# Kernel optimization log

Measured on AMD Instinct MI355X. Metric: run time of the kernel, lower is better.

The kernel has to match this reference:

```python
import jax, jax.numpy as jnp
import numpy as np

HIDDEN = 512

def setup_inputs() -> dict:
    key = jax.random.key(0)
    kx, kq, kk, kv = jax.random.split(key, 4)
    B, S, H = 4, 4096, HIDDEN
    scale = 1.0 / np.sqrt(H)
    x = jax.random.normal(kx, (B, S, H), dtype=jnp.float32)
    # nn.Linear weights are [out, in]; y = x @ W.T
    Wq = jax.random.normal(kq, (H, H), dtype=jnp.float32) * scale
    Wk = jax.random.normal(kk, (H, H), dtype=jnp.float32) * scale
    Wv = jax.random.normal(kv, (H, H), dtype=jnp.float32) * scale
    return {"x": x, "Wq": Wq, "Wk": Wk, "Wv": Wv}

def reference(x, Wq, Wk, Wv):
    H = x.shape[-1]
    q = jnp.einsum('bsh,oh->bso', x, Wq)
    k = jnp.einsum('bsh,oh->bso', x, Wk)
    v = jnp.einsum('bsh,oh->bso', x, Wv)
    scores = jnp.einsum('bqh,bkh->bqk', q, k) / jnp.sqrt(jnp.asarray(H, x.dtype))
    att = jax.nn.softmax(scores, axis=-1)  # max-subtracted softmax, same math as manual version
    return jnp.einsum('bqk,bkh->bqh', att, v)
```

## Files before the change

kernel.cpp:

```cpp
#include <hip/hip_runtime.h>
#include <stdint.h>

typedef unsigned short u16;
typedef __bf16  bf16x8   __attribute__((ext_vector_type(8)));
typedef float   floatx4  __attribute__((ext_vector_type(4)));
typedef unsigned short ushortx4 __attribute__((ext_vector_type(4)));

__device__ __forceinline__ u16 f2bf(float f) {
  unsigned u = __builtin_bit_cast(unsigned, f);
  u += 0x7FFFu + ((u >> 16) & 1u);
  return (u16)(u >> 16);
}

#define GLD_LDS16(g, l)                                                        \
  __builtin_amdgcn_global_load_lds(                                            \
      (const __attribute__((address_space(1))) void*)(g),                      \
      (__attribute__((address_space(3))) void*)(l), 16, 0, 0)

__global__ __launch_bounds__(256) void cvt_w(
    const float* __restrict__ Wq, const float* __restrict__ Wk,
    const float* __restrict__ Wv, u16* __restrict__ dst)
{
  const int z = blockIdx.y;
  const float* src = (z == 0) ? Wq : (z == 1) ? Wk : Wv;
  u16* d = dst + (size_t)z * 262144;
  const int idx = (blockIdx.x * 256 + threadIdx.x) * 8;
  const float4 lo = *(const float4*)&src[idx];
  const float4 hi = *(const float4*)&src[idx + 4];
  union { u16 h[8]; uint4 v; } pk;
  pk.h[0] = f2bf(lo.x); pk.h[1] = f2bf(lo.y); pk.h[2] = f2bf(lo.z); pk.h[3] = f2bf(lo.w);
  pk.h[4] = f2bf(hi.x); pk.h[5] = f2bf(hi.y); pk.h[6] = f2bf(hi.z); pk.h[7] = f2bf(hi.w);
  *(uint4*)&d[idx] = pk.v;
}

__global__ __launch_bounds__(256) void cvt_x(
    const float* __restrict__ X, u16* __restrict__ dst)
{
  const int idx = (blockIdx.x * 256 + threadIdx.x) * 8;
  const float4 lo = *(const float4*)&X[idx];
  const float4 hi = *(const float4*)&X[idx + 4];
  union { u16 h[8]; uint4 v; } pk;
  pk.h[0] = f2bf(lo.x); pk.h[1] = f2bf(lo.y); pk.h[2] = f2bf(lo.z); pk.h[3] = f2bf(lo.w);
  pk.h[4] = f2bf(hi.x); pk.h[5] = f2bf(hi.y); pk.h[6] = f2bf(hi.z); pk.h[7] = f2bf(hi.w);
  *(uint4*)&dst[idx] = pk.v;
}

__global__ __launch_bounds__(256, 2) void qkv_gemm(
    const u16* __restrict__ X16, const u16* __restrict__ Wb,
    u16* __restrict__ qo, u16* __restrict__ ko, u16* __restrict__ vto)
{
  __shared__ u16 As[128 * 32];
  __shared__ u16 Bs[128 * 32];

  const int tid = threadIdx.x;
  const int w  = tid >> 6, l = tid & 63;
  const int lr = l & 15, lq = l >> 4;
  const int lk = lq * 8;
  const int m0 = blockIdx.x * 128;
  const int n0 = blockIdx.y * 128;
  const int z  = blockIdx.z;
  const u16* W = Wb + (size_t)z * 262144;
  const int wm = (w & 1) * 64, wn = (w >> 1) * 64;

  floatx4 acc[4][4];
  const floatx4 fz = {0.f, 0.f, 0.f, 0.f};
#pragma unroll
  for (int i = 0; i < 4; ++i)
#pragma unroll
    for (int j = 0; j < 4; ++j) acc[i][j] = fz;

  for (int kk = 0; kk < 512; kk += 32) {
    __syncthreads();
#pragma unroll
    for (int i = 0; i < 2; ++i) {
      const int c = i * 256 + tid;
      const int row = c >> 2, c8 = (c & 3) * 8;
      GLD_LDS16(X16 + (size_t)(m0 + row) * 512 + kk + c8, &As[c * 8]);
      GLD_LDS16(W   + (size_t)(n0 + row) * 512 + kk + c8, &Bs[c * 8]);
    }
    __syncthreads();

    bf16x8 af[4], bfr[4];
#pragma unroll
    for (int t = 0; t < 4; ++t) {
      af[t]  = *(const bf16x8*)&As[(wm + t * 16 + lr) * 32 + lk];
      bfr[t] = *(const bf16x8*)&Bs[(wn + t * 16 + lr) * 32 + lk];
    }
#pragma unroll
    for (int i = 0; i < 4; ++i)
#pragma unroll
      for (int j = 0; j < 4; ++j)
        acc[i][j] = __builtin_amdgcn_mfma_f32_16x16x32_bf16(af[i], bfr[j],
                                                            acc[i][j], 0, 0, 0);
  }

  const int cr = lq * 4;
  if (z == 2) {
#pragma unroll
    for (int i = 0; i < 4; ++i)
#pragma unroll
      for (int j = 0; j < 4; ++j) {
        const int n = n0 + wn + j * 16 + lr;
        const int m = m0 + wm + i * 16 + cr;
        ushortx4 pk;
#pragma unroll
        for (int r = 0; r < 4; ++r) pk[r] = f2bf(acc[i][j][r]);
        *(ushortx4*)&vto[(size_t)n * 16384 + m] = pk;
      }
  } else {
    u16* dst = (z == 0) ? qo : ko;
    const float sc = (z == 0) ? 0.06375871732f : 1.0f;
#pragma unroll
    for (int i = 0; i < 4; ++i)
#pragma unroll
      for (int j = 0; j < 4; ++j) {
        const int m = m0 + wm + i * 16 + cr;
        const int n = n0 + wn + j * 16 + lr;
#pragma unroll
        for (int r = 0; r < 4; ++r)
          dst[(size_t)(m + r) * 512 + n] = f2bf(acc[i][j][r] * sc);
      }
  }
}

__global__ __launch_bounds__(256, 2) void qk_exp(
    const u16* __restrict__ q, const u16* __restrict__ k,
    u16* __restrict__ S, float* __restrict__ lsum)
{
  __shared__ u16 As[128 * 32];
  __shared__ u16 Bs[128 * 32];

  const int tid = threadIdx.x;
  const int w  = tid >> 6, l = tid & 63;
  const int lr = l & 15, lq = l >> 4;
  const int lk = lq * 8;
  const int m0 = blockIdx.x * 128;
  const int n0 = blockIdx.y * 128;
  const int b  = blockIdx.z;
  const int wm = (w & 1) * 64, wn = (w >> 1) * 64;
  const size_t rb = (size_t)b * 4096;

  floatx4 acc[4][4];
  const floatx4 fz = {0.f, 0.f, 0.f, 0.f};
#pragma unroll
  for (int i = 0; i < 4; ++i)
#pragma unroll
    for (int j = 0; j < 4; ++j) acc[i][j] = fz;

  for (int kk = 0; kk < 512; kk += 32) {
    __syncthreads();
#pragma unroll
    for (int i = 0; i < 2; ++i) {
      const int c = i * 256 + tid;
      const int row = c >> 2, c8 = (c & 3) * 8;
      GLD_LDS16(k + (rb + n0 + row) * 512 + kk + c8, &As[c * 8]);
      GLD_LDS16(q + (rb + m0 + row) * 512 + kk + c8, &Bs[c * 8]);
    }
    __syncthreads();

    bf16x8 af[4], bfr[4];
#pragma unroll
    for (int t = 0; t < 4; ++t) {
      af[t]  = *(const bf16x8*)&As[(wm + t * 16 + lr) * 32 + lk];
      bfr[t] = *(const bf16x8*)&Bs[(wn + t * 16 + lr) * 32 + lk];
    }
#pragma unroll
    for (int i = 0; i < 4; ++i)
#pragma unroll
      for (int j = 0; j < 4; ++j)
        acc[i][j] = __builtin_amdgcn_mfma_f32_16x16x32_bf16(af[i], bfr[j],
                                                            acc[i][j], 0, 0, 0);
  }

  const int cr = lq * 4;
  u16* Sb = S + ((size_t)b << 24);
  float js[4] = {0.f, 0.f, 0.f, 0.f};
#pragma unroll
  for (int i = 0; i < 4; ++i)
#pragma unroll
    for (int j = 0; j < 4; ++j) {
      const int key = n0 + wm + i * 16 + cr;
      const int qr  = m0 + wn + j * 16 + lr;
      ushortx4 pk;
      float s4 = 0.f;
#pragma unroll
      for (int r = 0; r < 4; ++r) {
        const float p = __builtin_amdgcn_exp2f(acc[i][j][r] - 17.31234049f);
        s4 += p;
        pk[r] = f2bf(p);
      }
      js[j] += s4;
      *(ushortx4*)&Sb[(size_t)qr * 4096 + key] = pk;
    }
#pragma unroll
  for (int j = 0; j < 4; ++j) {
    float s = js[j];
    s += __shfl_xor(s, 16);
    s += __shfl_xor(s, 32);
    if (lq == 0)
      atomicAdd(&lsum[rb + m0 + wn + j * 16 + lr], s);
  }
}

__global__ __launch_bounds__(256, 2) void pv(
    const u16* __restrict__ S, const u16* __restrict__ vt,
    const float* __restrict__ lsum, float* __restrict__ out)
{
  __shared__ u16 As[128 * 32];
  __shared__ u16 Bs[128 * 32];

  const int tid = threadIdx.x;
  const int w  = tid >> 6, l = tid & 63;
  const int lr = l & 15, lq = l >> 4;
  const int lk = lq * 8;

  const int wg = blockIdx.x;
  const int li = (wg & 7) * 64 + (wg >> 3);
  const int n0 = (li & 3) * 128;
  const int m0 = ((li >> 2) & 31) * 128;
  const int b  = li >> 7;
  const int wm = (w & 1) * 64, wn = (w >> 1) * 64;
  const u16* Sb = S + ((size_t)b << 24);

  floatx4 acc[4][4];
  const floatx4 fz = {0.f, 0.f, 0.f, 0.f};
#pragma unroll
  for (int i = 0; i < 4; ++i)
#pragma unroll
    for (int j = 0; j < 4; ++j) acc[i][j] = fz;

  for (int kk = 0; kk < 4096; kk += 32) {
    __syncthreads();
#pragma unroll
    for (int i = 0; i < 2; ++i) {
      const int c = i * 256 + tid;
      const int row = c >> 2, c8 = (c & 3) * 8;
      GLD_LDS16(Sb + (size_t)(m0 + row) * 4096 + kk + c8, &As[c * 8]);
      GLD_LDS16(vt + (size_t)(n0 + row) * 16384 + b * 4096 + kk + c8, &Bs[c * 8]);
    }
    __syncthreads();

    bf16x8 af[4], bfr[4];
#pragma unroll
    for (int t = 0; t < 4; ++t) {
      af[t]  = *(const bf16x8*)&As[(wm + t * 16 + lr) * 32 + lk];
      bfr[t] = *(const bf16x8*)&Bs[(wn + t * 16 + lr) * 32 + lk];
    }
#pragma unroll
    for (int i = 0; i < 4; ++i)
#pragma unroll
      for (int j = 0; j < 4; ++j)
        acc[i][j] = __builtin_amdgcn_mfma_f32_16x16x32_bf16(af[i], bfr[j],
                                                            acc[i][j], 0, 0, 0);
  }

  const int cr = lq * 4;
#pragma unroll
  for (int i = 0; i < 4; ++i) {
    const int m = m0 + wm + i * 16 + cr;
    float inv[4];
#pragma unroll
    for (int r = 0; r < 4; ++r)
      inv[r] = 1.0f / lsum[(size_t)b * 4096 + m + r];
#pragma unroll
    for (int j = 0; j < 4; ++j) {
      const int n = n0 + wn + j * 16 + lr;
#pragma unroll
      for (int r = 0; r < 4; ++r)
        out[((size_t)b * 4096 + m + r) * 512 + n] = acc[i][j][r] * inv[r];
    }
  }
}

extern "C" void kernel_launch(void* const* d_in, const int* in_sizes, int n_in,
                              void* d_out, int out_size, void* d_ws, size_t ws_size,
                              hipStream_t stream) {
  (void)in_sizes; (void)n_in; (void)out_size; (void)ws_size;
  const float* x  = (const float*)d_in[0];
  const float* Wq = (const float*)d_in[1];
  const float* Wk = (const float*)d_in[2];
  const float* Wv = (const float*)d_in[3];
  float* out = (float*)d_out;
  u16* ws  = (u16*)d_ws;
  u16* qw  = ws;
  u16* kw  = qw + (size_t)16384 * 512;
  u16* vw  = kw + (size_t)16384 * 512;
  u16* x16 = vw + (size_t)16384 * 512;
  u16* wb  = x16 + (size_t)16384 * 512;
  u16* Sp  = wb + (size_t)3 * 262144;
  float* lsum = (float*)(Sp + ((size_t)4 << 24));

  hipMemsetAsync(lsum, 0, 16384 * sizeof(float), stream);
  cvt_w<<<dim3(128, 3), dim3(256), 0, stream>>>(Wq, Wk, Wv, wb);
  cvt_x<<<dim3(4096), dim3(256), 0, stream>>>(x, x16);
  qkv_gemm<<<dim3(128, 4, 3), dim3(256), 0, stream>>>(x16, wb, qw, kw, vw);
  qk_exp<<<dim3(32, 32, 4), dim3(256), 0, stream>>>(qw, kw, Sp, lsum);
  pv<<<dim3(512), dim3(256), 0, stream>>>(Sp, vw, lsum, out);
}
```

Measured before the change: 310.2 us.

## Rewrite QK-exp kernel with 256x256 tiles, 8 waves, double-buffered swizzled LDS pipeline

The score kernel moves from 128x128 tiles with 4 waves and a load/sync/compute loop to 256x256 tiles with 8 waves. K and Q are streamed into a double-buffered, XOR-swizzled 128 KB LDS region, with loads issued several stages ahead and explicit vmcnt waits, barriers and setprio around the MFMA bursts. The aim is to hide global-load latency, avoid LDS bank conflicts and raise data reuse per loaded byte. The cost is much higher register (32 accumulators) and LDS use, which lowers occupancy, and a fragile hand-written wait/barrier schedule.

```diff
diff --git a/kernel.cpp b/kernel.cpp
--- a/kernel.cpp
+++ b/kernel.cpp
@@ -123,82 +123,138 @@
   }
 }
 
-__global__ __launch_bounds__(256, 2) void qk_exp(
+__global__ __launch_bounds__(512, 2) void qk_exp8(
     const u16* __restrict__ q, const u16* __restrict__ k,
     u16* __restrict__ S, float* __restrict__ lsum)
 {
-  __shared__ u16 As[128 * 32];
-  __shared__ u16 Bs[128 * 32];
+  __shared__ u16 lds[65536];
 
   const int tid = threadIdx.x;
   const int w  = tid >> 6, l = tid & 63;
   const int lr = l & 15, lq = l >> 4;
-  const int lk = lq * 8;
-  const int m0 = blockIdx.x * 128;
-  const int n0 = blockIdx.y * 128;
-  const int b  = blockIdx.z;
-  const int wm = (w & 1) * 64, wn = (w >> 1) * 64;
+  const int wA = (w & 1) * 16;
+  const int wB = (w >> 1) * 16;
+  const int kb0 = blockIdx.x * 256;
+  const int qb0 = blockIdx.y * 256;
+  const int b   = blockIdx.z;
   const size_t rb = (size_t)b * 4096;
-
-  floatx4 acc[4][4];
+  const u16* kg = k + rb * 512;
+  const u16* qg = q + rb * 512;
+
+  floatx4 acc[8][4];
   const floatx4 fz = {0.f, 0.f, 0.f, 0.f};
 #pragma unroll
-  for (int i = 0; i < 4; ++i)
+  for (int i = 0; i < 8; ++i)
 #pragma unroll
     for (int j = 0; j < 4; ++j) acc[i][j] = fz;
 
-  for (int kk = 0; kk < 512; kk += 32) {
-    __syncthreads();
+  auto stage = [&](int s) {
+    const int ts = s >> 2, kind = s & 3;
+    const int mat = kind & 1, h = kind >> 1;
+    const u16* src = mat ? qg : kg;
+    const int rbase = mat ? qb0 : kb0;
+    u16* dst = &lds[(ts & 1) * 32768 + mat * 16384];
 #pragma unroll
     for (int i = 0; i < 2; ++i) {
-      const int c = i * 256 + tid;
-      const int row = c >> 2, c8 = (c & 3) * 8;
-      GLD_LDS16(k + (rb + n0 + row) * 512 + kk + c8, &As[c * 8]);
-      GLD_LDS16(q + (rb + m0 + row) * 512 + kk + c8, &Bs[c * 8]);
-    }
-    __syncthreads();
-
-    bf16x8 af[4], bfr[4];
-#pragma unroll
-    for (int t = 0; t < 4; ++t) {
-      af[t]  = *(const bf16x8*)&As[(wm + t * 16 + lr) * 32 + lk];
-      bfr[t] = *(const bf16x8*)&Bs[(wn + t * 16 + lr) * 32 + lk];
-    }
-#pragma unroll
-    for (int i = 0; i < 4; ++i)
-#pragma unroll
-      for (int j = 0; j < 4; ++j)
-        acc[i][j] = __builtin_amdgcn_mfma_f32_16x16x32_bf16(af[i], bfr[j],
-                                                            acc[i][j], 0, 0, 0);
+      const int c = i * 512 + tid;
+      const int r = h * 128 + (c >> 3), k16 = c & 7;
+      const int k16s = k16 ^ (r & 7);
+      GLD_LDS16(src + (size_t)(rbase + r) * 512 + ts * 64 + k16s * 8,
+                &dst[r * 64 + k16 * 8]);
+    }
+  };
+
+#pragma unroll
+  for (int s = 0; s < 6; ++s) stage(s);
+  asm volatile("s_waitcnt vmcnt(4)" ::: "memory");
+  __builtin_amdgcn_s_barrier();
+  __builtin_amdgcn_sched_barrier(0);
+
+#pragma unroll
+  for (int t = 0; t < 8; ++t) {
+#pragma unroll
+    for (int qd = 0; qd < 4; ++qd) {
+      const int fmh = qd >> 1, fnh = qd & 1;
+      const u16* AB = &lds[(t & 1) * 32768];
+      const u16* BB = AB + 16384;
+
+      bf16x8 af[4][2], bfv[2][2];
+#pragma unroll
+      for (int im = 0; im < 4; ++im) {
+        const int rA = (fmh * 4 + im) * 32 + wA + lr;
+#pragma unroll
+        for (int ks = 0; ks < 2; ++ks) {
+          const int k16p = (ks * 4 + lq) ^ (rA & 7);
+          af[im][ks] = *(const bf16x8*)&AB[rA * 64 + k16p * 8];
+        }
+      }
+#pragma unroll
+      for (int jn = 0; jn < 2; ++jn) {
+        const int rB = (fnh * 2 + jn) * 64 + wB + lr;
+#pragma unroll
+        for (int ks = 0; ks < 2; ++ks) {
+          const int k16p = (ks * 4 + lq) ^ (rB & 7);
+          bfv[jn][ks] = *(const bf16x8*)&BB[rB * 64 + k16p * 8];
+        }
+      }
+
+      const int s = t * 4 + qd + 6;
+      if (s < 32) stage(s);
+
+      __builtin_amdgcn_sched_barrier(0);
+      __builtin_amdgcn_s_barrier();
+      asm volatile("s_waitcnt lgkmcnt(0)" ::: "memory");
+      __builtin_amdgcn_sched_barrier(0);
+
+      __builtin_amdgcn_s_setprio(1);
+#pragma unroll
+      for (int im = 0; im < 4; ++im)
+#pragma unroll
+        for (int jn = 0; jn < 2; ++jn)
+#pragma unroll
+          for (int ks = 0; ks < 2; ++ks)
+            acc[fmh * 4 + im][fnh * 2 + jn] =
+                __builtin_amdgcn_mfma_f32_16x16x32_bf16(
+                    af[im][ks], bfv[jn][ks],
+                    acc[fmh * 4 + im][fnh * 2 + jn], 0, 0, 0);
+      __builtin_amdgcn_s_setprio(0);
+
+      if (qd == 3) {
+        if (t < 6)        asm volatile("s_waitcnt vmcnt(4)" ::: "memory");
+        else if (t == 6)  asm volatile("s_waitcnt vmcnt(0)" ::: "memory");
+      }
+      __builtin_amdgcn_s_barrier();
+      __builtin_amdgcn_sched_barrier(0);
+    }
   }
 
   const int cr = lq * 4;
   u16* Sb = S + ((size_t)b << 24);
   float js[4] = {0.f, 0.f, 0.f, 0.f};
 #pragma unroll
-  for (int i = 0; i < 4; ++i)
-#pragma unroll
-    for (int j = 0; j < 4; ++j) {
-      const int key = n0 + wm + i * 16 + cr;
-      const int qr  = m0 + wn + j * 16 + lr;
+  for (int fm = 0; fm < 8; ++fm)
+#pragma unroll
+    for (int fn = 0; fn < 4; ++fn) {
+      const int key = kb0 + fm * 32 + wA + cr;
+      const int qr  = qb0 + fn * 64 + wB + lr;
       ushortx4 pk;
       float s4 = 0.f;
 #pragma unroll
       for (int r = 0; r < 4; ++r) {
-        const float p = __builtin_amdgcn_exp2f(acc[i][j][r] - 17.31234049f);
+        const float p = __builtin_amdgcn_exp2f(acc[fm][fn][r] - 17.31234049f);
         s4 += p;
         pk[r] = f2bf(p);
       }
-      js[j] += s4;
+      js[fn] += s4;
       *(ushortx4*)&Sb[(size_t)qr * 4096 + key] = pk;
     }
 #pragma unroll
-  for (int j = 0; j < 4; ++j) {
-    float s = js[j];
+  for (int fn = 0; fn < 4; ++fn) {
+    float s = js[fn];
     s += __shfl_xor(s, 16);
     s += __shfl_xor(s, 32);
     if (lq == 0)
-      atomicAdd(&lsum[rb + m0 + wn + j * 16 + lr], s);
+      atomicAdd(&lsum[rb + qb0 + fn * 64 + wB + lr], s);
   }
 }
 
@@ -294,6 +350,6 @@
   cvt_w<<<dim3(128, 3), dim3(256), 0, stream>>>(Wq, Wk, Wv, wb);
   cvt_x<<<dim3(4096), dim3(256), 0, stream>>>(x, x16);
   qkv_gemm<<<dim3(128, 4, 3), dim3(256), 0, stream>>>(x16, wb, qw, kw, vw);
-  qk_exp<<<dim3(32, 32, 4), dim3(256), 0, stream>>>(qw, kw, Sp, lsum);
+  qk_exp8<<<dim3(16, 16, 4), dim3(512), 0, stream>>>(qw, kw, Sp, lsum);
   pv<<<dim3(512), dim3(256), 0, stream>>>(Sp, vw, lsum, out);
 }
```

Measured after the change: 319.4 us. +3.0%, slower.
